# Kernel tuning notes

Measured on AMD Instinct MI355X. Metric: run time of the kernel, lower is better.

## Reference

```python
import jax, jax.numpy as jnp
import numpy as np

EPS = 1e-12


def setup_inputs() -> dict:
    key = jax.random.key(0)
    n, k, Eu, iterations = 200_000, 7, 1_600_000, 3
    k1, k2, k3 = jax.random.split(key, 3)
    # undirected edge list; each undirected edge yields two directed edges
    su = jax.random.randint(k1, (Eu,), 0, n, dtype=jnp.int32)
    du = jax.random.randint(k2, (Eu,), 0, n, dtype=jnp.int32)
    src = jnp.concatenate([su, du])                                   # [E]
    dst = jnp.concatenate([du, su])                                   # [E]
    rev = jnp.concatenate([jnp.arange(Eu, 2 * Eu, dtype=jnp.int32),
                           jnp.arange(Eu, dtype=jnp.int32)])          # [E]
    # node priors (rows sum to 1), mimicking the soft label priors
    prior = jax.random.uniform(k3, (n, k), minval=0.1, maxval=1.0)
    prior = prior / prior.sum(axis=1, keepdims=True)
    # label-to-label potential: log(beta) on the diagonal (beta = 3.0)
    W = jnp.log(3.0) * jnp.eye(k, dtype=jnp.float32)
    return {"prior": prior, "W": W, "src": src, "dst": dst,
            "rev": rev, "iterations": iterations}


def reference(prior, W, src, dst, rev, iterations):
    n, k = prior.shape
    E = src.shape[0]
    psi = jnp.exp(jnp.clip(W, -10.0, 10.0))                           # [k,k]
    msgs = jnp.full((E, k), 1.0 / k, dtype=prior.dtype)

    def step(msgs, _):
        # product of incoming messages per node, in log-space (msgs >= EPS)
        logm = jnp.log(msgs)                                          # [E,k]
        logP = jax.ops.segment_sum(logm, dst, num_segments=n)         # [n,k]
        # per directed edge (i -> j): remove reverse message j -> i
        prod_in_i = jnp.exp(logP[src] - logm[rev])                    # [E,k]
        b = jnp.maximum(prior[src] * prod_in_i, EPS)                  # [E,k]
        m_new = jnp.maximum(b @ psi, EPS)                             # [E,k]
        m_new = m_new / jnp.maximum(m_new.sum(-1, keepdims=True), EPS)
        return m_new, None

    msgs, _ = jax.lax.scan(step, msgs, None, length=int(iterations))

    # beliefs
    logP = jax.ops.segment_sum(jnp.log(msgs), dst, num_segments=n)    # [n,k]
    b = jnp.maximum(prior * jnp.exp(logP), EPS)
    return b / jnp.maximum(b.sum(-1, keepdims=True), EPS)
```

## Files before the change

### kernel.cpp

```cpp
#include <hip/hip_runtime.h>
#include <hip/hip_bf16.h>
#include <hip/hip_fp16.h>

#define K 7
#define EPSF 1e-12f
#define LOG_INV_K (-1.9459101090932196f)
#define LOG7 1.9459101090932196f
#define LOG2_EPS (-39.8631371f)
#define LN2 0.69314718056f
#define INV_LN2 1.44269504f
#define SBN 512
#define SBSH 9
#define NSBMAX 768
#define PB 256

__device__ __forceinline__ float ldf(const void* p, size_t idx, int mode) {
    return mode ? ((const float*)p)[idx]
                : __bfloat162float(((const __hip_bfloat16*)p)[idx]);
}

__device__ __forceinline__ void load_psi(const void* W, float* psi, int mode) {
    if (threadIdx.x < K * K) {
        float w = ldf(W, threadIdx.x, mode);
        w = fminf(fmaxf(w, -10.f), 10.f);
        psi[threadIdx.x] = __expf(w);
    }
    __syncthreads();
}

__device__ __forceinline__ void bp_lin(const float* b, const float* psi, float* m) {
    float o[K], sum = 0.f;
#pragma unroll
    for (int j = 0; j < K; j++) {
        float acc = 0.f;
#pragma unroll
        for (int i = 0; i < K; i++) acc += b[i] * psi[i * K + j];
        o[j] = fmaxf(acc, EPSF);
        sum += o[j];
    }
    float inv = __fdividef(1.f, fmaxf(sum, EPSF));
#pragma unroll
    for (int j = 0; j < K; j++) m[j] = o[j] * inv;
}

__device__ __forceinline__ void acc_log_msg(const float* b, const float* psi, float* acc) {
    float m[K];
    bp_lin(b, psi, m);
#pragma unroll
    for (int j = 0; j < K; j++) acc[j] += __logf(m[j]);
}

__device__ __forceinline__ void ld8(const float* base, float* r) {
    const float4* p = (const float4*)base;
    float4 a = p[0], b = p[1];
    r[0]=a.x; r[1]=a.y; r[2]=a.z; r[3]=a.w; r[4]=b.x; r[5]=b.y; r[6]=b.z; r[7]=b.w;
}

__device__ __forceinline__ void dec_pd(uint4 w, float* p, int* degv, int* u1) {
    p[0] = __uint_as_float((w.x & 0xffffu) << 16);
    p[1] = __uint_as_float(w.x & 0xffff0000u);
    p[2] = __uint_as_float((w.y & 0xffffu) << 16);
    p[3] = __uint_as_float(w.y & 0xffff0000u);
    p[4] = __uint_as_float((w.z & 0xffffu) << 16);
    p[5] = __uint_as_float(w.z & 0xffff0000u);
    p[6] = __uint_as_float((w.w & 0xffffu) << 16);
    *degv = (int)((w.w >> 16) & 0x7fffu);
    *u1 = (int)(w.w >> 31);
}

__device__ __forceinline__ unsigned short f2h(float f) {
    __half h = __float2half_rn(f);
    return *reinterpret_cast<unsigned short*>(&h);
}
__device__ __forceinline__ float h2f(unsigned short u) {
    __half h;
    *reinterpret_cast<unsigned short*>(&h) = u;
    return __half2float(h);
}
__device__ __forceinline__ uint4 pack7h(const float* m, int E) {
    uint4 r;
    r.x = (unsigned)f2h(m[0]) | ((unsigned)f2h(m[1]) << 16);
    r.y = (unsigned)f2h(m[2]) | ((unsigned)f2h(m[3]) << 16);
    r.z = (unsigned)f2h(m[4]) | ((unsigned)f2h(m[5]) << 16);
    r.w = (unsigned)f2h(m[6]) | ((unsigned)(E & 0xffff) << 16);
    return r;
}
__device__ __forceinline__ int unpack7h(uint4 w, float* m) {
    m[0] = h2f((unsigned short)(w.x & 0xffffu));
    m[1] = h2f((unsigned short)(w.x >> 16));
    m[2] = h2f((unsigned short)(w.y & 0xffffu));
    m[3] = h2f((unsigned short)(w.y >> 16));
    m[4] = h2f((unsigned short)(w.z & 0xffffu));
    m[5] = h2f((unsigned short)(w.z >> 16));
    m[6] = h2f((unsigned short)(w.w & 0xffffu));
    return (int)(short)(w.w >> 16);
}

__global__ void sniff8_kernel(const void* __restrict__ W, int* __restrict__ prm) {
    if (blockIdx.x != 0 || threadIdx.x != 0) return;
    const unsigned int* Wraw = (const unsigned int*)W;
    int mode = ((Wraw[0] >> 16) != 0u) ? 1 : 0;
    float diag0 = 0.f, offd0 = 0.f;
    int structured = 1;
    for (int i = 0; i < K; i++)
        for (int j = 0; j < K; j++) {
            float w = ldf(W, i * K + j, mode);
            w = fminf(fmaxf(w, -10.f), 10.f);
            float e = __expf(w);
            if (i == 0 && j == 0) diag0 = e;
            if (i == 0 && j == 1) offd0 = e;
            if (i == j) { if (i > 0 && e != diag0) structured = 0; }
            else       { if (!(i == 0 && j == 1) && e != offd0) structured = 0; }
        }
    if (!(offd0 >= 0.2f) || !(diag0 >= offd0)) structured = 0;
    prm[0] = mode | (structured << 1);
    ((float*)prm)[1] = offd0;
    ((float*)prm)[2] = diag0;
}

__global__ void hist6_kernel(const int* __restrict__ dst, int* __restrict__ hist,
                             int* __restrict__ btot, int E, int EPB, int NSB) {
    __shared__ int h[NSBMAX];
    for (int i = threadIdx.x; i < NSB; i += 256) h[i] = 0;
    __syncthreads();
    int blk = blockIdx.x;
    int e0 = blk * EPB, e1 = min(e0 + EPB, E);
    for (int e = e0 + (int)threadIdx.x; e < e1; e += 256)
        atomicAdd(&h[dst[e] >> SBSH], 1);
    __syncthreads();
    for (int i = threadIdx.x; i < NSB; i += 256) {
        int c = h[i];
        hist[i * PB + blk] = c;
        if (c) atomicAdd(&btot[i], c);
    }
}

__global__ void bscan6_kernel(const int* __restrict__ btot, int* __restrict__ boff, int NSB) {
    __shared__ int s[1024];
    int t = threadIdx.x;
    int x = (t < NSB) ? btot[t] : 0;
    s[t] = x;
    __syncthreads();
    for (int o = 1; o < 1024; o <<= 1) {
        int y = (t >= o) ? s[t - o] : 0;
        __syncthreads();
        s[t] += y;
        __syncthreads();
    }
    if (t < NSB) boff[t] = s[t] - x;
    if (t == NSB - 1) boff[NSB] = s[t];
}

__global__ void sscan6_kernel(const int* __restrict__ hist, const int* __restrict__ boff,
                              int* __restrict__ woff) {
    __shared__ int s[PB];
    int b = blockIdx.x, t = threadIdx.x;
    int x = hist[b * PB + t];
    s[t] = x;
    __syncthreads();
    for (int o = 1; o < PB; o <<= 1) {
        int y = (t >= o) ? s[t - o] : 0;
        __syncthreads();
        s[t] += y;
        __syncthreads();
    }
    woff[b * PB + t] = boff[b] + s[t] - x;
}

__global__ void part6_kernel(const int* __restrict__ src, const int* __restrict__ dst,
                             const int* __restrict__ woff, unsigned int* __restrict__ coarse,
                             int E, int EPB, int NSB) {
    __shared__ int cur[NSBMAX];
    int blk = blockIdx.x;
    for (int i = threadIdx.x; i < NSB; i += 256) cur[i] = woff[i * PB + blk];
    __syncthreads();
    int e0 = blk * EPB, e1 = min(e0 + EPB, E);
    for (int e = e0 + (int)threadIdx.x; e < e1; e += 256) {
        int d = dst[e];
        int b = d >> SBSH;
        unsigned int pk = (unsigned int)src[e] | ((unsigned int)(d & (SBN - 1)) << 18);
        int pos = atomicAdd(&cur[b], 1);
        coarse[pos] = pk;
    }
}

__global__ void cfill9_kernel(const unsigned int* __restrict__ coarse,
                              const int* __restrict__ boff,
                              const void* __restrict__ prior, const int* __restrict__ prm,
                              int* __restrict__ cur, int* __restrict__ nbr,
                              uint4* __restrict__ PD, int n) {
    __shared__ int lcnt[SBN], lcur[SBN];
    int b = blockIdx.x, t = threadIdx.x;
    int mode = prm[0] & 1;
    for (int i = t; i < SBN; i += 256) lcnt[i] = 0;
    __syncthreads();
    int s0 = boff[b], s1 = boff[b + 1];
    for (int i = s0 + t; i < s1; i += 256)
        atomicAdd(&lcnt[coarse[i] >> 18], 1);
    __syncthreads();
    if (t == 0) {
        int a = s0;
        for (int l = 0; l < SBN; l++) { lcur[l] = a; a += lcnt[l]; }
    }
    __syncthreads();
    int v0 = b << SBSH;
    for (int i = t; i < SBN; i += 256) {
        int v = v0 + i;
        if (v >= n) continue;
        int degv = lcnt[i];
        cur[v] = lcur[i] + degv;
        unsigned int pb[K];
        float p[K];
        if (mode == 0) {
            const unsigned short* pr = (const unsigned short*)prior;
#pragma unroll
            for (int j = 0; j < K; j++) {
                pb[j] = pr[(size_t)v * K + j];
                p[j] = __uint_as_float(pb[j] << 16);
            }
        } else {
            const float* pr = (const float*)prior;
#pragma unroll
            for (int j = 0; j < K; j++) {
                p[j] = pr[(size_t)v * K + j];
                __hip_bfloat16 hh = __float2bfloat16(p[j]);
                pb[j] = *(unsigned short*)&hh;
            }
        }
        float es = __expf((float)(degv - 1) * LOG_INV_K);
        float mx = p[0];
#pragma unroll
        for (int j = 1; j < K; j++) mx = fmaxf(mx, p[j]);
        unsigned int u1 = (mx * es <= EPSF) ? 1u : 0u;
        int dcap = degv > 0x7fff ? 0x7fff : degv;
        uint4 w;
        w.x = pb[0] | (pb[1] << 16);
        w.y = pb[2] | (pb[3] << 16);
        w.z = pb[4] | (pb[5] << 16);
        w.w = pb[6] | (((unsigned int)dcap) << 16) | (u1 << 31);
        PD[v] = w;
    }
    __syncthreads();
    for (int i = s0 + t; i < s1; i += 256) {
        unsigned int w = coarse[i];
        int pos = atomicAdd(&lcur[w >> 18], 1);
        nbr[pos] = (int)(w & 0x3FFFFu);
    }
}

__global__ void mbuild10_kernel(const uint4* __restrict__ PD, const void* __restrict__ W,
                                const int* __restrict__ prm, uint4* __restrict__ R32, int n) {
    __shared__ float psi[K * K];
    int pm = prm[0];
    int mode = pm & 1, strq = (pm >> 1) & 1;
    float offd = ((const float*)prm)[1], diag = ((const float*)prm)[2];
    load_psi(W, psi, mode);
    int v = blockIdx.x * blockDim.x + threadIdx.x;
    if (v >= n) return;
    float p[K]; int dv, u1v;
    dec_pd(PD[v], p, &dv, &u1v);
    float es = __expf((float)(dv - 1) * LOG_INV_K);
    float b[K], S = 0.f;
#pragma unroll
    for (int i = 0; i < K; i++) { b[i] = fmaxf(p[i] * es, EPSF); S += b[i]; }
    float m1n[K];
    if (strq) {
        float cb = diag - offd, norm = 6.f * offd + diag;
        float sc = __fdividef(7.f, S * norm);
#pragma unroll
        for (int i = 0; i < K; i++) m1n[i] = (offd * S + cb * b[i]) * sc;
    } else {
        float m1[K];
        bp_lin(b, psi, m1);
#pragma unroll
        for (int i = 0; i < K; i++) m1n[i] = 7.f * m1[i];
    }
    R32[2 * (size_t)v] = pack7h(m1n, 0);
}

__global__ void n2v10_kernel(const int* __restrict__ cur, const int* __restrict__ nbr,
                             const uint4* __restrict__ R32, const uint4* __restrict__ PD,
                             const int* __restrict__ prm, uint4* __restrict__ LP1,
                             float* __restrict__ EP1f, int n) {
    int t = blockIdx.x * blockDim.x + threadIdx.x;
    int v = t >> 2, qi = t & 3;
    if (v >= n) return;
    int start = v ? cur[v - 1] : 0, end = cur[v];
    int len = end - start;
    int lo = start + ((len * qi) >> 2), hi = start + ((len * (qi + 1)) >> 2);
    float acc[K] = {1.f, 1.f, 1.f, 1.f, 1.f, 1.f, 1.f};
    int e = lo;
    for (; e + 1 < hi; e += 2) {
        int ua = nbr[e], ub = nbr[e + 1];
        uint4 wa = R32[2 * (size_t)ua];
        uint4 wb = R32[2 * (size_t)ub];
        float a[K], c[K];
        unpack7h(wa, a);
        unpack7h(wb, c);
#pragma unroll
        for (int i = 0; i < K; i++) acc[i] *= a[i] * c[i];
    }
    if (e < hi) {
        float a[K];
        unpack7h(R32[2 * (size_t)nbr[e]], a);
#pragma unroll
        for (int i = 0; i < K; i++) acc[i] *= a[i];
    }
#pragma unroll
    for (int i = 0; i < K; i++) {
        acc[i] *= __shfl_xor(acc[i], 1, 64);
        acc[i] *= __shfl_xor(acc[i], 2, 64);
    }
    if (qi) return;
    float pv[K]; int dv, u1v;
    dec_pd(PD[v], pv, &dv, &u1v);
    float le[K], mx = -1e30f;
    float corr = (float)len * LOG7;
#pragma unroll
    for (int i = 0; i < K; i++) {
        le[i] = __logf(pv[i] * acc[i]) - corr;
        mx = fmaxf(mx, le[i]);
    }
    int E1 = (int)ceilf(mx * INV_LN2);
    float fm[K];
#pragma unroll
    for (int i = 0; i < K; i++) fm[i] = __expf(le[i] - (float)E1 * LN2);
    LP1[v] = pack7h(fm, E1);
    float4* q = (float4*)(EP1f + (size_t)v * 8);
    q[0] = make_float4(ldexpf(fm[0], E1), ldexpf(fm[1], E1), ldexpf(fm[2], E1), ldexpf(fm[3], E1));
    q[1] = make_float4(ldexpf(fm[4], E1), ldexpf(fm[5], E1), ldexpf(fm[6], E1), 0.f);
}

__global__ void n3v10_kernel(const int* __restrict__ cur, const int* __restrict__ nbr,
                             const uint4* __restrict__ PD, const uint4* __restrict__ LP1,
                             const void* __restrict__ W, const int* __restrict__ prm,
                             uint4* __restrict__ R32, int n) {
    __shared__ float psi[K * K];
    int pm = prm[0];
    int mode = pm & 1, strq = (pm >> 1) & 1;
    float offd = ((const float*)prm)[1], diag = ((const float*)prm)[2];
    load_psi(W, psi, mode);
    int t = blockIdx.x * blockDim.x + threadIdx.x;
    int v = t >> 2, qi = t & 3;
    if (v >= n) return;
    int start = v ? cur[v - 1] : 0, end = cur[v];
    int len = end - start;
    int lo = start + ((len * qi) >> 2), hi = start + ((len * (qi + 1)) >> 2);
    float cb = diag - offd, norm = 6.f * offd + diag;
    float pv[K]; int dv, u1v;
    dec_pd(PD[v], pv, &dv, &u1v);
    float rm1v[K], mrv = 0.f;
    if (strq && u1v) {
#pragma unroll
        for (int i = 0; i < K; i++) rm1v[i] = 7.f;
        mrv = 7.f;
    } else {
        float es = __expf((float)(dv - 1) * LOG_INV_K);
        float b1[K], S1 = 0.f;
#pragma unroll
        for (int i = 0; i < K; i++) { b1[i] = fmaxf(pv[i] * es, EPSF); S1 += b1[i]; }
        if (strq) {
            float inv = __fdividef(1.f, S1 * norm);
#pragma unroll
            for (int i = 0; i < K; i++) {
                float m1 = (offd * S1 + cb * b1[i]) * inv;
                rm1v[i] = __fdividef(1.f, m1);
                mrv = fmaxf(mrv, rm1v[i]);
            }
        } else {
            float m1[K];
            bp_lin(b1, psi, m1);
#pragma unroll
            for (int i = 0; i < K; i++) rm1v[i] = __fdividef(1.f, m1[i]);
        }
    }
    float acc[K];
    int cn = 0;
    if (strq) {
        int Ethr = (int)floorf(LOG2_EPS - log2f(mrv));
#pragma unroll
        for (int i = 0; i < K; i++) acc[i] = 1.f;
        auto proc = [&](uint4 q) {
            float m[K];
            int E = unpack7h(q, m);
            if (E <= Ethr) return;
            float b[K], S = 0.f;
#pragma unroll
            for (int i = 0; i < K; i++) {
                b[i] = fmaxf(ldexpf(m[i] * rm1v[i], E), EPSF);
                S += b[i];
            }
            float crS = __fdividef(cb, S);
#pragma unroll
            for (int i = 0; i < K; i++) acc[i] *= fmaf(crS, b[i], offd);
            cn++;
        };
        int e = lo;
        for (; e + 1 < hi; e += 2) {
            int ua = nbr[e], ub = nbr[e + 1];
            uint4 qa = LP1[ua], qb = LP1[ub];
            proc(qa);
            proc(qb);
        }
        if (e < hi) proc(LP1[nbr[e]]);
#pragma unroll
        for (int i = 0; i < K; i++) {
            acc[i] *= __shfl_xor(acc[i], 1, 64);
            acc[i] *= __shfl_xor(acc[i], 2, 64);
        }
    } else {
#pragma unroll
        for (int i = 0; i < K; i++) acc[i] = 0.f;
        for (int e = lo; e < hi; e++) {
            float m[K];
            int E = unpack7h(LP1[nbr[e]], m);
            float b[K];
#pragma unroll
            for (int i = 0; i < K; i++)
                b[i] = fmaxf(ldexpf(m[i] * rm1v[i], E), EPSF);
            acc_log_msg(b, psi, acc);
        }
#pragma unroll
        for (int i = 0; i < K; i++) {
            acc[i] += __shfl_xor(acc[i], 1, 64);
            acc[i] += __shfl_xor(acc[i], 2, 64);
        }
    }
    cn += __shfl_xor(cn, 1, 64);
    cn += __shfl_xor(cn, 2, 64);
    if (qi) return;
    float le2[K], mx = -1e30f;
    if (strq) {
        float corr = (float)cn * __logf(norm) + (float)(len - cn) * LOG7;
#pragma unroll
        for (int i = 0; i < K; i++) {
            le2[i] = __logf(pv[i] * acc[i]) - corr;
            mx = fmaxf(mx, le2[i]);
        }
    } else {
#pragma unroll
        for (int i = 0; i < K; i++) {
            le2[i] = __logf(pv[i]) + acc[i];
            mx = fmaxf(mx, le2[i]);
        }
    }
    int E2 = (int)ceilf(mx * INV_LN2);
    float fm[K];
#pragma unroll
    for (int i = 0; i < K; i++) fm[i] = __expf(le2[i] - (float)E2 * LN2);
    R32[2 * (size_t)v + 1] = pack7h(fm, E2);
}

__global__ void n4v10_kernel(const int* __restrict__ cur, const int* __restrict__ nbr,
                             const uint4* __restrict__ R32, const float* __restrict__ EP1f,
                             const void* __restrict__ prior, const void* __restrict__ W,
                             const int* __restrict__ prm, void* __restrict__ out, int n) {
    __shared__ float psi[K * K];
    int pm = prm[0];
    int mode = pm & 1, strq = (pm >> 1) & 1;
    float offd = ((const float*)prm)[1], diag = ((const float*)prm)[2];
    load_psi(W, psi, mode);
    int t = blockIdx.x * blockDim.x + threadIdx.x;
    int v = t >> 2, qi = t & 3;
    if (v >= n) return;
    int start = v ? cur[v - 1] : 0, end = cur[v];
    int len = end - start;
    int lo = start + ((len * qi) >> 2), hi = start + ((len * (qi + 1)) >> 2);
    float cb = diag - offd, norm = 6.f * offd + diag;
    float e1v[8];
    ld8(EP1f + (size_t)v * 8, e1v);
    float acc[K];
    int cn = 0;
    if (strq) {
        float mx1 = e1v[0];
#pragma unroll
        for (int i = 1; i < K; i++) mx1 = fmaxf(mx1, e1v[i]);
        float F = __fdividef(norm, offd) * 1.01f;
        int m2u = (F * mx1 <= EPSF);
        int Ethr2 = (int)floorf(LOG2_EPS - log2f(7.f));
        int Ethr3 = (int)floorf(LOG2_EPS - log2f(F));
#pragma unroll
        for (int i = 0; i < K; i++) acc[i] = 1.f;
        if (m2u) {
            auto proc = [&](uint4 q) {
                float m[K];
                int E2 = unpack7h(q, m);
                if (E2 <= Ethr2) return;
                float b3[K], S = 0.f;
#pragma unroll
                for (int i = 0; i < K; i++) {
                    b3[i] = fmaxf(ldexpf(m[i] * 7.f, E2), EPSF);
                    S += b3[i];
                }
                float crS = __fdividef(cb, S);
#pragma unroll
                for (int i = 0; i < K; i++) acc[i] *= fmaf(crS, b3[i], offd);
                cn++;
            };
            int e = lo;
            for (; e + 1 < hi; e += 2) {
                int ua = nbr[e], ub = nbr[e + 1];
                uint4 qa = R32[2 * (size_t)ua + 1];
                uint4 qb = R32[2 * (size_t)ub + 1];
                proc(qa);
                proc(qb);
            }
            if (e < hi) proc(R32[2 * (size_t)nbr[e] + 1]);
        } else {
            for (int e = lo; e < hi; e++) {
                size_t u = (size_t)nbr[e];
                uint4 q = R32[2 * u + 1];
                float m[K];
                int E2 = unpack7h(q, m);
                if (E2 <= Ethr3) continue;
                float tt[K];
                unpack7h(R32[2 * u], tt);
                float b2[K], S2 = 0.f;
#pragma unroll
                for (int i = 0; i < K; i++) {
                    b2[i] = fmaxf(e1v[i] * __fdividef(7.f, tt[i]), EPSF);
                    S2 += b2[i];
                }
                float inv2 = __fdividef(1.f, S2 * norm);
                float b3[K], S3 = 0.f;
#pragma unroll
                for (int i = 0; i < K; i++) {
                    float m2v = (offd * S2 + cb * b2[i]) * inv2;
                    float e2 = ldexpf(m[i], E2);
                    b3[i] = fmaxf(__fdividef(e2, m2v), EPSF);
                    S3 += b3[i];
                }
                float crS3 = __fdividef(cb, S3);
#pragma unroll
                for (int i = 0; i < K; i++) acc[i] *= fmaf(crS3, b3[i], offd);
                cn++;
            }
        }
#pragma unroll
        for (int i = 0; i < K; i++) {
            acc[i] *= __shfl_xor(acc[i], 1, 64);
            acc[i] *= __shfl_xor(acc[i], 2, 64);
        }
    } else {
#pragma unroll
        for (int i = 0; i < K; i++) acc[i] = 0.f;
        for (int e = lo; e < hi; e++) {
            size_t u = (size_t)nbr[e];
            uint4 q = R32[2 * u + 1];
            float m[K];
            int E2 = unpack7h(q, m);
            float tt[K];
            unpack7h(R32[2 * u], tt);
            float b2[K];
#pragma unroll
            for (int i = 0; i < K; i++)
                b2[i] = fmaxf(e1v[i] * __fdividef(7.f, tt[i]), EPSF);
            float m2[K];
            bp_lin(b2, psi, m2);
            float b3[K];
#pragma unroll
            for (int i = 0; i < K; i++) {
                float e2 = ldexpf(m[i], E2);
                b3[i] = fmaxf(__fdividef(e2, m2[i]), EPSF);
            }
            acc_log_msg(b3, psi, acc);
        }
#pragma unroll
        for (int i = 0; i < K; i++) {
            acc[i] += __shfl_xor(acc[i], 1, 64);
            acc[i] += __shfl_xor(acc[i], 2, 64);
        }
    }
    cn += __shfl_xor(cn, 1, 64);
    cn += __shfl_xor(cn, 2, 64);
    if (qi) return;
    float bb[K], sum = 0.f;
    if (strq) {
        float corr = (float)cn * __logf(norm) + (float)(len - cn) * LOG7;
#pragma unroll
        for (int i = 0; i < K; i++) {
            float p = ldf(prior, (size_t)v * K + i, mode);
            bb[i] = fmaxf(__expf(__logf(p * acc[i]) - corr), EPSF);
            sum += bb[i];
        }
    } else {
#pragma unroll
        for (int i = 0; i < K; i++) {
            float p = ldf(prior, (size_t)v * K + i, mode);
            bb[i] = fmaxf(p * __expf(acc[i]), EPSF);
            sum += bb[i];
        }
    }
    float inv = __fdividef(1.f, fmaxf(sum, EPSF));
#pragma unroll
    for (int i = 0; i < K; i++) {
        float val = bb[i] * inv;
        if (mode) ((float*)out)[(size_t)v * K + i] = val;
        else ((__hip_bfloat16*)out)[(size_t)v * K + i] = __float2bfloat16(val);
    }
}

__device__ __forceinline__ void bp_msg(const float* b, const float* psi, float* lm) {
    float m[K];
    bp_lin(b, psi, m);
#pragma unroll
    for (int j = 0; j < K; j++) lm[j] = __logf(m[j]);
}
__device__ __forceinline__ void msg1(const void* prior, int node, int degv, int mode,
                                     const float* psi, float* lm) {
    float es = __expf((float)(degv - 1) * LOG_INV_K);
    float b[K];
#pragma unroll
    for (int i = 0; i < K; i++)
        b[i] = fmaxf(ldf(prior, (size_t)node * K + i, mode) * es, EPSF);
    bp_msg(b, psi, lm);
}
__device__ __forceinline__ void msgF(const void* prior, int node,
                                     const float* __restrict__ logP,
                                     const float* lmrev, int mode,
                                     const float* psi, float* lm) {
    float b[K];
#pragma unroll
    for (int i = 0; i < K; i++)
        b[i] = fmaxf(ldf(prior, (size_t)node * K + i, mode) *
                     __expf(logP[(size_t)node * K + i] - lmrev[i]), EPSF);
    bp_msg(b, psi, lm);
}
__global__ void deg_kernel(const int* __restrict__ su, const int* __restrict__ du,
                           int* __restrict__ deg, int Eu) {
    int u = blockIdx.x * blockDim.x + threadIdx.x;
    if (u >= Eu) return;
    atomicAdd(&deg[su[u]], 1);
    atomicAdd(&deg[du[u]], 1);
}
__global__ void pass1_kernel(const int* __restrict__ su, const int* __restrict__ du,
                             const int* __restrict__ deg, const void* __restrict__ prior,
                             const void* __restrict__ W, const int* __restrict__ prm,
                             float* __restrict__ logP1, int Eu) {
    __shared__ float psi[K * K];
    int mode = prm[0] & 1;
    load_psi(W, psi, mode);
    int u = blockIdx.x * blockDim.x + threadIdx.x;
    if (u >= Eu) return;
    int s = su[u], d = du[u];
    float lm[K];
    msg1(prior, s, deg[s], mode, psi, lm);
#pragma unroll
    for (int j = 0; j < K; j++) atomicAdd(&logP1[(size_t)d * K + j], lm[j]);
    msg1(prior, d, deg[d], mode, psi, lm);
#pragma unroll
    for (int j = 0; j < K; j++) atomicAdd(&logP1[(size_t)s * K + j], lm[j]);
}
__global__ void pass2_kernel(const int* __restrict__ su, const int* __restrict__ du,
                             const int* __restrict__ deg, const void* __restrict__ prior,
                             const void* __restrict__ W, const int* __restrict__ prm,
                             const float* __restrict__ logP1, float* __restrict__ logP2, int Eu) {
    __shared__ float psi[K * K];
    int mode = prm[0] & 1;
    load_psi(W, psi, mode);
    int u = blockIdx.x * blockDim.x + threadIdx.x;
    if (u >= Eu) return;
    int s = su[u], d = du[u];
    float lm1sd[K], lm1ds[K], lm[K];
    msg1(prior, s, deg[s], mode, psi, lm1sd);
    msg1(prior, d, deg[d], mode, psi, lm1ds);
    msgF(prior, s, logP1, lm1ds, mode, psi, lm);
#pragma unroll
    for (int j = 0; j < K; j++) atomicAdd(&logP2[(size_t)d * K + j], lm[j]);
    msgF(prior, d, logP1, lm1sd, mode, psi, lm);
#pragma unroll
    for (int j = 0; j < K; j++) atomicAdd(&logP2[(size_t)s * K + j], lm[j]);
}
__global__ void pass3_kernel(const int* __restrict__ su, const int* __restrict__ du,
                             const int* __restrict__ deg, const void* __restrict__ prior,
                             const void* __restrict__ W, const int* __restrict__ prm,
                             const float* __restrict__ logP1, const float* __restrict__ logP2,
                             float* __restrict__ logP3, int Eu) {
    __shared__ float psi[K * K];
    int mode = prm[0] & 1;
    load_psi(W, psi, mode);
    int u = blockIdx.x * blockDim.x + threadIdx.x;
    if (u >= Eu) return;
    int s = su[u], d = du[u];
    float lm1sd[K], lm1ds[K], lm2sd[K], lm2ds[K], lm[K];
    msg1(prior, s, deg[s], mode, psi, lm1sd);
    msg1(prior, d, deg[d], mode, psi, lm1ds);
    msgF(prior, s, logP1, lm1ds, mode, psi, lm2sd);
    msgF(prior, d, logP1, lm1sd, mode, psi, lm2ds);
    msgF(prior, s, logP2, lm2ds, mode, psi, lm);
#pragma unroll
    for (int j = 0; j < K; j++) atomicAdd(&logP3[(size_t)d * K + j], lm[j]);
    msgF(prior, d, logP2, lm2sd, mode, psi, lm);
#pragma unroll
    for (int j = 0; j < K; j++) atomicAdd(&logP3[(size_t)s * K + j], lm[j]);
}
__global__ void belief_kernel(const float* __restrict__ logP3, const void* __restrict__ prior,
                              const int* __restrict__ prm, void* __restrict__ out, int n) {
    int v = blockIdx.x * blockDim.x + threadIdx.x;
    if (v >= n) return;
    int mode = prm[0] & 1;
    float b[K], sum = 0.f;
#pragma unroll
    for (int j = 0; j < K; j++) {
        b[j] = fmaxf(ldf(prior, (size_t)v * K + j, mode) * __expf(logP3[(size_t)v * K + j]), EPSF);
        sum += b[j];
    }
    float inv = __fdividef(1.f, fmaxf(sum, EPSF));
#pragma unroll
    for (int j = 0; j < K; j++) {
        float val = b[j] * inv;
        if (mode) ((float*)out)[(size_t)v * K + j] = val;
        else ((__hip_bfloat16*)out)[(size_t)v * K + j] = __float2bfloat16(val);
    }
}

extern "C" void kernel_launch(void* const* d_in, const int* in_sizes, int n_in,
                              void* d_out, int out_size, void* d_ws, size_t ws_size,
                              hipStream_t stream) {
    const void* prior = d_in[0];
    const void* W     = d_in[1];
    const int* src = (const int*)d_in[2];
    const int* dst = (const int*)d_in[3];

    int n  = in_sizes[0] / K;
    int E  = in_sizes[2];
    int Eu = E / 2;

    const int B = 256;
    int gn  = (n + B - 1) / B;
    int gn4 = (4 * n + B - 1) / B;
    int ge  = (Eu + B - 1) / B;

    int NSB = (n + SBN - 1) >> SBSH;
    int EPB = (E + PB - 1) / PB;

    char* ws = (char*)d_ws;
    size_t off = 0;
    auto alloc = [&](size_t bytes) { size_t o = off; off = (off + bytes + 127) & ~(size_t)127; return o; };

    size_t xsz = (size_t)E * 4;
    if ((size_t)n * 48 > xsz) xsz = (size_t)n * 48;
    size_t o_nbr  = alloc((size_t)E * 4);
    size_t o_X    = alloc(xsz);
    size_t o_PD   = alloc((size_t)n * 16);
    size_t o_EP1f = alloc((size_t)n * 32);
    size_t o_cur  = alloc((size_t)n * 4);
    size_t o_hist = alloc((size_t)NSB * PB * 4);
    size_t o_woff = alloc((size_t)NSB * PB * 4);
    size_t o_boff = alloc((size_t)(NSB + 1) * 4);
    size_t o_btot = alloc((size_t)NSB * 4);
    size_t o_prm  = alloc(64);
    size_t need_v10 = off;

    bool v10_ok = (ws_size >= need_v10) && (n <= (1 << 18)) && (NSB <= NSBMAX) && (NSB >= 1);

    if (v10_ok) {
        int*   nbr    = (int*)(ws + o_nbr);
        unsigned int* coarse = (unsigned int*)(ws + o_X);
        uint4* LP1    = (uint4*)(ws + o_X);
        uint4* R32    = (uint4*)(ws + o_X + (size_t)n * 16);
        uint4* PD     = (uint4*)(ws + o_PD);
        float* EP1f   = (float*)(ws + o_EP1f);
        int*   cur    = (int*)(ws + o_cur);
        int*   hist   = (int*)(ws + o_hist);
        int*   woff   = (int*)(ws + o_woff);
        int*   boff   = (int*)(ws + o_boff);
        int*   btot   = (int*)(ws + o_btot);
        int*   prm    = (int*)(ws + o_prm);

        sniff8_kernel<<<1, 64, 0, stream>>>(W, prm);
        hipMemsetAsync(btot, 0, (size_t)NSB * 4, stream);
        hist6_kernel<<<PB, B, 0, stream>>>(dst, hist, btot, E, EPB, NSB);
        bscan6_kernel<<<1, 1024, 0, stream>>>(btot, boff, NSB);
        sscan6_kernel<<<NSB, PB, 0, stream>>>(hist, boff, woff);
        part6_kernel<<<PB, B, 0, stream>>>(src, dst, woff, coarse, E, EPB, NSB);
        cfill9_kernel<<<NSB, B, 0, stream>>>(coarse, boff, prior, prm, cur, nbr, PD, n);
        mbuild10_kernel<<<gn, B, 0, stream>>>(PD, W, prm, R32, n);
        n2v10_kernel<<<gn4, B, 0, stream>>>(cur, nbr, R32, PD, prm, LP1, EP1f, n);
        n3v10_kernel<<<gn4, B, 0, stream>>>(cur, nbr, PD, LP1, W, prm, R32, n);
        n4v10_kernel<<<gn4, B, 0, stream>>>(cur, nbr, R32, EP1f, prior, W, prm, d_out, n);
        return;
    }

    {
        float* logP1 = (float*)d_ws;
        float* logP2 = logP1 + (size_t)n * K;
        float* logP3 = logP2 + (size_t)n * K;
        int*   deg   = (int*)(logP3 + (size_t)n * K);
        int*   prm   = deg + n;
        sniff8_kernel<<<1, 64, 0, stream>>>(W, prm);
        hipMemsetAsync(d_ws, 0, ((size_t)3 * n * K + n) * sizeof(float), stream);
        deg_kernel<<<ge, B, 0, stream>>>(src, dst, deg, Eu);
        pass1_kernel<<<ge, B, 0, stream>>>(src, dst, deg, prior, W, prm, logP1, Eu);
        pass2_kernel<<<ge, B, 0, stream>>>(src, dst, deg, prior, W, prm, logP1, logP2, Eu);
        pass3_kernel<<<ge, B, 0, stream>>>(src, dst, deg, prior, W, prm, logP1, logP2, logP3, Eu);
        belief_kernel<<<gn, B, 0, stream>>>(logP3, prior, prm, d_out, n);
    }
}
```

Baseline: 318.5 us.

## Split interleaved message buffer, drop fp32 EP1 array, unroll gathers by four

The interleaved R32 buffer becomes two contiguous 16-byte-per-node arrays (M1h and Q2h), so each gather loads from a dense array instead of a strided one. The fp32 EP1f side array is removed, and n4 rebuilds those values from the packed LP1 with ldexpf. That saves a write and a read of 32 bytes per node. Neighbour gather loops in n2, n3 and n4 are unrolled from two to four to keep more loads in flight, and the btot memset is folded into the sniff kernel to save a launch. Small clamps are added before logs and divides for robustness, which adds a few extra ALU operations.

```diff
diff --git a/kernel.cpp b/kernel.cpp
--- a/kernel.cpp
+++ b/kernel.cpp
@@ -50,12 +50,6 @@
     for (int j = 0; j < K; j++) acc[j] += __logf(m[j]);
 }
 
-__device__ __forceinline__ void ld8(const float* base, float* r) {
-    const float4* p = (const float4*)base;
-    float4 a = p[0], b = p[1];
-    r[0]=a.x; r[1]=a.y; r[2]=a.z; r[3]=a.w; r[4]=b.x; r[5]=b.y; r[6]=b.z; r[7]=b.w;
-}
-
 __device__ __forceinline__ void dec_pd(uint4 w, float* p, int* degv, int* u1) {
     p[0] = __uint_as_float((w.x & 0xffffu) << 16);
     p[1] = __uint_as_float(w.x & 0xffff0000u);
@@ -96,8 +90,11 @@
     return (int)(short)(w.w >> 16);
 }
 
-__global__ void sniff8_kernel(const void* __restrict__ W, int* __restrict__ prm) {
-    if (blockIdx.x != 0 || threadIdx.x != 0) return;
+__global__ void sniff11_kernel(const void* __restrict__ W, int* __restrict__ prm,
+                               int* __restrict__ btot, int NSB) {
+    if (blockIdx.x != 0) return;
+    for (int i = threadIdx.x; i < NSB; i += 64) btot[i] = 0;
+    if (threadIdx.x != 0) return;
     const unsigned int* Wraw = (const unsigned int*)W;
     int mode = ((Wraw[0] >> 16) != 0u) ? 1 : 0;
     float diag0 = 0.f, offd0 = 0.f;
@@ -248,8 +245,8 @@
     }
 }
 
-__global__ void mbuild10_kernel(const uint4* __restrict__ PD, const void* __restrict__ W,
-                                const int* __restrict__ prm, uint4* __restrict__ R32, int n) {
+__global__ void mbuild11_kernel(const uint4* __restrict__ PD, const void* __restrict__ W,
+                                const int* __restrict__ prm, uint4* __restrict__ M1h, int n) {
     __shared__ float psi[K * K];
     int pm = prm[0];
     int mode = pm & 1, strq = (pm >> 1) & 1;
@@ -275,13 +272,12 @@
 #pragma unroll
         for (int i = 0; i < K; i++) m1n[i] = 7.f * m1[i];
     }
-    R32[2 * (size_t)v] = pack7h(m1n, 0);
-}
-
-__global__ void n2v10_kernel(const int* __restrict__ cur, const int* __restrict__ nbr,
-                             const uint4* __restrict__ R32, const uint4* __restrict__ PD,
-                             const int* __restrict__ prm, uint4* __restrict__ LP1,
-                             float* __restrict__ EP1f, int n) {
+    M1h[v] = pack7h(m1n, 0);
+}
+
+__global__ void n2v11_kernel(const int* __restrict__ cur, const int* __restrict__ nbr,
+                             const uint4* __restrict__ M1h, const uint4* __restrict__ PD,
+                             const int* __restrict__ prm, uint4* __restrict__ LP1, int n) {
     int t = blockIdx.x * blockDim.x + threadIdx.x;
     int v = t >> 2, qi = t & 3;
     if (v >= n) return;
@@ -290,21 +286,19 @@
     int lo = start + ((len * qi) >> 2), hi = start + ((len * (qi + 1)) >> 2);
     float acc[K] = {1.f, 1.f, 1.f, 1.f, 1.f, 1.f, 1.f};
     int e = lo;
-    for (; e + 1 < hi; e += 2) {
-        int ua = nbr[e], ub = nbr[e + 1];
-        uint4 wa = R32[2 * (size_t)ua];
-        uint4 wb = R32[2 * (size_t)ub];
-        float a[K], c[K];
-        unpack7h(wa, a);
-        unpack7h(wb, c);
-#pragma unroll
-        for (int i = 0; i < K; i++) acc[i] *= a[i] * c[i];
-    }
-    if (e < hi) {
+    for (; e + 3 < hi; e += 4) {
+        int u0 = nbr[e], u1 = nbr[e + 1], u2 = nbr[e + 2], u3 = nbr[e + 3];
+        uint4 w0 = M1h[u0], w1 = M1h[u1], w2 = M1h[u2], w3 = M1h[u3];
+        float a[K], b[K], c[K], d[K];
+        unpack7h(w0, a); unpack7h(w1, b); unpack7h(w2, c); unpack7h(w3, d);
+#pragma unroll
+        for (int i = 0; i < K; i++) acc[i] *= (a[i] * b[i]) * (c[i] * d[i]);
+    }
+    for (; e < hi; e++) {
         float a[K];
-        unpack7h(R32[2 * (size_t)nbr[e]], a);
-#pragma unroll
-        for (int i = 0; i < K; i++) acc[i] *= a[i];
+        unpack7h(M1h[nbr[e]], a);
+#pragma unroll
+        for (int i = 0; i < K; i++) acc[i] *= fmaxf(a[i], 1e-30f);
     }
 #pragma unroll
     for (int i = 0; i < K; i++) {
@@ -318,7 +312,7 @@
     float corr = (float)len * LOG7;
 #pragma unroll
     for (int i = 0; i < K; i++) {
-        le[i] = __logf(pv[i] * acc[i]) - corr;
+        le[i] = __logf(fmaxf(pv[i] * acc[i], 1e-37f)) - corr;
         mx = fmaxf(mx, le[i]);
     }
     int E1 = (int)ceilf(mx * INV_LN2);
@@ -326,15 +320,12 @@
 #pragma unroll
     for (int i = 0; i < K; i++) fm[i] = __expf(le[i] - (float)E1 * LN2);
     LP1[v] = pack7h(fm, E1);
-    float4* q = (float4*)(EP1f + (size_t)v * 8);
-    q[0] = make_float4(ldexpf(fm[0], E1), ldexpf(fm[1], E1), ldexpf(fm[2], E1), ldexpf(fm[3], E1));
-    q[1] = make_float4(ldexpf(fm[4], E1), ldexpf(fm[5], E1), ldexpf(fm[6], E1), 0.f);
-}
-
-__global__ void n3v10_kernel(const int* __restrict__ cur, const int* __restrict__ nbr,
+}
+
+__global__ void n3v11_kernel(const int* __restrict__ cur, const int* __restrict__ nbr,
                              const uint4* __restrict__ PD, const uint4* __restrict__ LP1,
                              const void* __restrict__ W, const int* __restrict__ prm,
-                             uint4* __restrict__ R32, int n) {
+                             uint4* __restrict__ Q2h, int n) {
     __shared__ float psi[K * K];
     int pm = prm[0];
     int mode = pm & 1, strq = (pm >> 1) & 1;
@@ -396,13 +387,12 @@
             cn++;
         };
         int e = lo;
-        for (; e + 1 < hi; e += 2) {
-            int ua = nbr[e], ub = nbr[e + 1];
-            uint4 qa = LP1[ua], qb = LP1[ub];
-            proc(qa);
-            proc(qb);
-        }
-        if (e < hi) proc(LP1[nbr[e]]);
+        for (; e + 3 < hi; e += 4) {
+            int u0 = nbr[e], u1 = nbr[e + 1], u2 = nbr[e + 2], u3 = nbr[e + 3];
+            uint4 q0 = LP1[u0], q1 = LP1[u1], q2 = LP1[u2], q3 = LP1[u3];
+            proc(q0); proc(q1); proc(q2); proc(q3);
+        }
+        for (; e < hi; e++) proc(LP1[nbr[e]]);
 #pragma unroll
         for (int i = 0; i < K; i++) {
             acc[i] *= __shfl_xor(acc[i], 1, 64);
@@ -434,13 +424,13 @@
         float corr = (float)cn * __logf(norm) + (float)(len - cn) * LOG7;
 #pragma unroll
         for (int i = 0; i < K; i++) {
-            le2[i] = __logf(pv[i] * acc[i]) - corr;
+            le2[i] = __logf(fmaxf(pv[i] * acc[i], 1e-37f)) - corr;
             mx = fmaxf(mx, le2[i]);
         }
     } else {
 #pragma unroll
         for (int i = 0; i < K; i++) {
-            le2[i] = __logf(pv[i]) + acc[i];
+            le2[i] = __logf(fmaxf(pv[i], 1e-37f)) + acc[i];
             mx = fmaxf(mx, le2[i]);
         }
     }
@@ -448,13 +438,14 @@
     float fm[K];
 #pragma unroll
     for (int i = 0; i < K; i++) fm[i] = __expf(le2[i] - (float)E2 * LN2);
-    R32[2 * (size_t)v + 1] = pack7h(fm, E2);
-}
-
-__global__ void n4v10_kernel(const int* __restrict__ cur, const int* __restrict__ nbr,
-                             const uint4* __restrict__ R32, const float* __restrict__ EP1f,
-                             const void* __restrict__ prior, const void* __restrict__ W,
-                             const int* __restrict__ prm, void* __restrict__ out, int n) {
+    Q2h[v] = pack7h(fm, E2);
+}
+
+__global__ void n4v11_kernel(const int* __restrict__ cur, const int* __restrict__ nbr,
+                             const uint4* __restrict__ M1h, const uint4* __restrict__ Q2h,
+                             const uint4* __restrict__ LP1, const void* __restrict__ prior,
+                             const void* __restrict__ W, const int* __restrict__ prm,
+                             void* __restrict__ out, int n) {
     __shared__ float psi[K * K];
     int pm = prm[0];
     int mode = pm & 1, strq = (pm >> 1) & 1;
@@ -467,8 +458,13 @@
     int len = end - start;
     int lo = start + ((len * qi) >> 2), hi = start + ((len * (qi + 1)) >> 2);
     float cb = diag - offd, norm = 6.f * offd + diag;
-    float e1v[8];
-    ld8(EP1f + (size_t)v * 8, e1v);
+    float e1v[K];
+    {
+        float m[K];
+        int E1 = unpack7h(LP1[v], m);
+#pragma unroll
+        for (int i = 0; i < K; i++) e1v[i] = ldexpf(m[i], E1);
+    }
     float acc[K];
     int cn = 0;
     if (strq) {
@@ -498,23 +494,21 @@
                 cn++;
             };
             int e = lo;
-            for (; e + 1 < hi; e += 2) {
-                int ua = nbr[e], ub = nbr[e + 1];
-                uint4 qa = R32[2 * (size_t)ua + 1];
-                uint4 qb = R32[2 * (size_t)ub + 1];
-                proc(qa);
-                proc(qb);
+            for (; e + 3 < hi; e += 4) {
+                int u0 = nbr[e], u1 = nbr[e + 1], u2 = nbr[e + 2], u3 = nbr[e + 3];
+                uint4 q0 = Q2h[u0], q1 = Q2h[u1], q2 = Q2h[u2], q3 = Q2h[u3];
+                proc(q0); proc(q1); proc(q2); proc(q3);
             }
-            if (e < hi) proc(R32[2 * (size_t)nbr[e] + 1]);
+            for (; e < hi; e++) proc(Q2h[nbr[e]]);
         } else {
             for (int e = lo; e < hi; e++) {
-                size_t u = (size_t)nbr[e];
-                uint4 q = R32[2 * u + 1];
+                int u = nbr[e];
+                uint4 q = Q2h[u];
                 float m[K];
                 int E2 = unpack7h(q, m);
                 if (E2 <= Ethr3) continue;
                 float tt[K];
-                unpack7h(R32[2 * u], tt);
+                unpack7h(M1h[u], tt);
                 float b2[K], S2 = 0.f;
 #pragma unroll
                 for (int i = 0; i < K; i++) {
@@ -545,16 +539,16 @@
 #pragma unroll
         for (int i = 0; i < K; i++) acc[i] = 0.f;
         for (int e = lo; e < hi; e++) {
-            size_t u = (size_t)nbr[e];
-            uint4 q = R32[2 * u + 1];
+            int u = nbr[e];
+            uint4 q = Q2h[u];
             float m[K];
             int E2 = unpack7h(q, m);
             float tt[K];
-            unpack7h(R32[2 * u], tt);
+            unpack7h(M1h[u], tt);
             float b2[K];
 #pragma unroll
             for (int i = 0; i < K; i++)
-                b2[i] = fmaxf(e1v[i] * __fdividef(7.f, tt[i]), EPSF);
+                b2[i] = fmaxf(e1v[i] * __fdividef(7.f, fmaxf(tt[i], 1e-30f)), EPSF);
             float m2[K];
             bp_lin(b2, psi, m2);
             float b3[K];
@@ -580,7 +574,7 @@
 #pragma unroll
         for (int i = 0; i < K; i++) {
             float p = ldf(prior, (size_t)v * K + i, mode);
-            bb[i] = fmaxf(__expf(__logf(p * acc[i]) - corr), EPSF);
+            bb[i] = fmaxf(__expf(__logf(fmaxf(p * acc[i], 1e-37f)) - corr), EPSF);
             sum += bb[i];
         }
     } else {
@@ -743,24 +737,23 @@
     size_t o_nbr  = alloc((size_t)E * 4);
     size_t o_X    = alloc(xsz);
     size_t o_PD   = alloc((size_t)n * 16);
-    size_t o_EP1f = alloc((size_t)n * 32);
     size_t o_cur  = alloc((size_t)n * 4);
     size_t o_hist = alloc((size_t)NSB * PB * 4);
     size_t o_woff = alloc((size_t)NSB * PB * 4);
     size_t o_boff = alloc((size_t)(NSB + 1) * 4);
     size_t o_btot = alloc((size_t)NSB * 4);
     size_t o_prm  = alloc(64);
-    size_t need_v10 = off;
-
-    bool v10_ok = (ws_size >= need_v10) && (n <= (1 << 18)) && (NSB <= NSBMAX) && (NSB >= 1);
-
-    if (v10_ok) {
+    size_t need_v11 = off;
+
+    bool v11_ok = (ws_size >= need_v11) && (n <= (1 << 18)) && (NSB <= NSBMAX) && (NSB >= 1);
+
+    if (v11_ok) {
         int*   nbr    = (int*)(ws + o_nbr);
         unsigned int* coarse = (unsigned int*)(ws + o_X);
         uint4* LP1    = (uint4*)(ws + o_X);
-        uint4* R32    = (uint4*)(ws + o_X + (size_t)n * 16);
+        uint4* Q2h    = (uint4*)(ws + o_X + (size_t)n * 16);
+        uint4* M1h    = (uint4*)(ws + o_X + (size_t)n * 32);
         uint4* PD     = (uint4*)(ws + o_PD);
-        float* EP1f   = (float*)(ws + o_EP1f);
         int*   cur    = (int*)(ws + o_cur);
         int*   hist   = (int*)(ws + o_hist);
         int*   woff   = (int*)(ws + o_woff);
@@ -768,17 +761,16 @@
         int*   btot   = (int*)(ws + o_btot);
         int*   prm    = (int*)(ws + o_prm);
 
-        sniff8_kernel<<<1, 64, 0, stream>>>(W, prm);
-        hipMemsetAsync(btot, 0, (size_t)NSB * 4, stream);
+        sniff11_kernel<<<1, 64, 0, stream>>>(W, prm, btot, NSB);
         hist6_kernel<<<PB, B, 0, stream>>>(dst, hist, btot, E, EPB, NSB);
         bscan6_kernel<<<1, 1024, 0, stream>>>(btot, boff, NSB);
         sscan6_kernel<<<NSB, PB, 0, stream>>>(hist, boff, woff);
         part6_kernel<<<PB, B, 0, stream>>>(src, dst, woff, coarse, E, EPB, NSB);
         cfill9_kernel<<<NSB, B, 0, stream>>>(coarse, boff, prior, prm, cur, nbr, PD, n);
-        mbuild10_kernel<<<gn, B, 0, stream>>>(PD, W, prm, R32, n);
-        n2v10_kernel<<<gn4, B, 0, stream>>>(cur, nbr, R32, PD, prm, LP1, EP1f, n);
-        n3v10_kernel<<<gn4, B, 0, stream>>>(cur, nbr, PD, LP1, W, prm, R32, n);
-        n4v10_kernel<<<gn4, B, 0, stream>>>(cur, nbr, R32, EP1f, prior, W, prm, d_out, n);
+        mbuild11_kernel<<<gn, B, 0, stream>>>(PD, W, prm, M1h, n);
+        n2v11_kernel<<<gn4, B, 0, stream>>>(cur, nbr, M1h, PD, prm, LP1, n);
+        n3v11_kernel<<<gn4, B, 0, stream>>>(cur, nbr, PD, LP1, W, prm, Q2h, n);
+        n4v11_kernel<<<gn4, B, 0, stream>>>(cur, nbr, M1h, Q2h, LP1, prior, W, prm, d_out, n);
         return;
     }
 
@@ -788,7 +780,8 @@
         float* logP3 = logP2 + (size_t)n * K;
         int*   deg   = (int*)(logP3 + (size_t)n * K);
         int*   prm   = deg + n;
-        sniff8_kernel<<<1, 64, 0, stream>>>(W, prm);
+        int*   btot  = prm + 8;
+        sniff11_kernel<<<1, 64, 0, stream>>>(W, prm, btot, 0);
         hipMemsetAsync(d_ws, 0, ((size_t)3 * n * K + n) * sizeof(float), stream);
         deg_kernel<<<ge, B, 0, stream>>>(src, dst, deg, Eu);
         pass1_kernel<<<ge, B, 0, stream>>>(src, dst, deg, prior, W, prm, logP1, Eu);
```

After: 294.2 us. -7.6%, faster.
